# Kernel optimization log

Measured on AMD Instinct MI355X. Metric: run time of the kernel, lower is better.

## Reference

```python
import jax, jax.numpy as jnp
import numpy as np

N, E, G, DIM = 100000, 1600000, 64, 128
BN_EPS = 1e-5


def setup_inputs() -> dict:
    key = jax.random.key(0)
    ks = jax.random.split(key, 20)
    inp = {
        "x": jax.random.normal(ks[0], (N, DIM), jnp.float32),
        "edge_attr": jax.random.normal(ks[1], (E, DIM), jnp.float32),
        "u": jax.random.normal(ks[2], (G, DIM), jnp.float32),
        "edge_index": jax.random.randint(ks[3], (2, E), 0, N, jnp.int32),
        "batch": jnp.sort(jax.random.randint(ks[4], (N,), 0, G, jnp.int32)),
    }
    # MLP params: layer 0 is Linear(3*DIM, DIM), layers 1,2 are Linear(DIM, DIM)
    def xavier(k, shape):
        fan_in, fan_out = shape[1], shape[0]
        lim = jnp.sqrt(6.0 / (fan_in + fan_out))
        return jax.random.uniform(k, shape, jnp.float32, -lim, lim)
    inp["W0"] = xavier(ks[5], (DIM, 3 * DIM)); inp["b0"] = jnp.zeros((DIM,), jnp.float32)
    inp["W1"] = xavier(ks[6], (DIM, DIM));     inp["b1"] = jnp.zeros((DIM,), jnp.float32)
    inp["W2"] = xavier(ks[7], (DIM, DIM));     inp["b2"] = jnp.zeros((DIM,), jnp.float32)
    for i in range(3):
        inp[f"g{i}"] = jnp.ones((DIM,), jnp.float32)   # BN gamma
        inp[f"bt{i}"] = jnp.zeros((DIM,), jnp.float32)  # BN beta
    return inp


def _bn(h, gamma, beta):
    # training-mode BatchNorm1d: batch mean, biased variance
    mu = jnp.mean(h, axis=0)
    var = jnp.var(h, axis=0)
    return (h - mu) * jax.lax.rsqrt(var + BN_EPS) * gamma + beta


def reference(x, edge_attr, u, W0, b0, W1, b1, W2, b2,
              g0, bt0, g1, bt1, g2, bt2, edge_index, batch):
    n = x.shape[0]
    src = edge_index[0]
    # scatter_mean(edge_attr, src) -> [N, DIM]
    sums = jax.ops.segment_sum(edge_attr, src, num_segments=n)
    cnt = jax.ops.segment_sum(jnp.ones((edge_attr.shape[0],), edge_attr.dtype),
                              src, num_segments=n)
    v_e = sums / jnp.maximum(cnt, 1.0)[:, None]
    out = jnp.concatenate([x, v_e, u[batch]], axis=1)  # [N, 3*DIM]
    for W, b, g, bt in ((W0, b0, g0, bt0), (W1, b1, g1, bt1), (W2, b2, g2, bt2)):
        out = jax.nn.relu(out @ W.T + b)
        out = _bn(out, g, bt)
        # dropout_rate = 0.0 -> identity
    return out
```

## Files before the change

kernel.cpp:

```cpp
#include <hip/hip_runtime.h>

#define DIMF 128
#define CAP 128

typedef __bf16 bf16x8 __attribute__((ext_vector_type(8)));
typedef float f32x4 __attribute__((ext_vector_type(4)));
typedef float f32x2 __attribute__((ext_vector_type(2)));

__device__ __forceinline__ unsigned short f2bf(float f) {
    union { float f; unsigned u; } v; v.f = f;
    unsigned r = v.u + 0x7FFFu + ((v.u >> 16) & 1u);
    return (unsigned short)(r >> 16);
}
__device__ __forceinline__ float bf2f(unsigned short h) {
    union { unsigned u; float f; } v; v.u = ((unsigned)h) << 16; return v.f;
}

__global__ __launch_bounds__(256) void k_zero_wconv(int* __restrict__ zbase, int zints,
                                                    const float* __restrict__ W, unsigned short* __restrict__ Wb,
                                                    int n4) {
    int idx = blockIdx.x * 256 + threadIdx.x;
    int z0 = idx * 2;
    if (z0 + 1 < zints) {
        *reinterpret_cast<int2*>(zbase + z0) = int2{0, 0};
    } else if (z0 < zints) {
        zbase[z0] = 0;
    }
    if (idx < n4) {
        float4 v = *reinterpret_cast<const float4*>(W + (size_t)idx * 4);
        ushort4 o = { f2bf(v.x), f2bf(v.y), f2bf(v.z), f2bf(v.w) };
        *reinterpret_cast<ushort4*>(Wb + (size_t)idx * 4) = o;
    }
}

__global__ __launch_bounds__(256) void k_fillb(const int* __restrict__ src, int* __restrict__ cnt,
                                               int* __restrict__ order, int E) {
    int e = blockIdx.x * 256 + threadIdx.x;
    if (e < E) {
        int s = src[e];
        int p = atomicAdd(&cnt[s], 1);
        if (p < CAP) order[(size_t)s * CAP + p] = e;
    }
}

__global__ __launch_bounds__(256) void k_gather(const float* __restrict__ ea, const int* __restrict__ order,
                                                const int* __restrict__ cnt,
                                                unsigned short* __restrict__ ve, int n) {
    int node = blockIdx.x * 4 + (threadIdx.x >> 6);
    if (node >= n) return;
    int lane = threadIdx.x & 63;
    int half = lane >> 5;
    int l32 = lane & 31;
    int c = cnt[node];
    if (c > CAP) c = CAP;
    size_t base = (size_t)node * CAP;

    int id0 = (lane < c) ? order[base + lane] : 0;
    int id1 = (c > 64 && lane < c - 64) ? order[base + 64 + lane] : 0;

    int m  = (c > half) ? ((c - half + 1) >> 1) : 0;
    int mu = (c + 1) >> 1;

#define EID(t) ({ int j_ = half + 2 * (t); \
                  (j_ < 64) ? __shfl(id0, j_, 64) : __shfl(id1, j_ - 64, 64); })
#define LDR(eid) __builtin_nontemporal_load(reinterpret_cast<const f32x4*>(ea + (size_t)(eid) * DIMF) + l32)

    f32x4 s = {0.f, 0.f, 0.f, 0.f};
    f32x4 cur[4], nxt[4];
    int tb = mu >> 2;
    if (tb > 0) {
#pragma unroll
        for (int k = 0; k < 4; ++k) cur[k] = LDR(EID(k));
        for (int b = 1; b < tb; ++b) {
#pragma unroll
            for (int k = 0; k < 4; ++k) nxt[k] = LDR(EID(b * 4 + k));
#pragma unroll
            for (int k = 0; k < 4; ++k) {
                int t = (b - 1) * 4 + k;
                if (t < m) s += cur[k];
                cur[k] = nxt[k];
            }
        }
#pragma unroll
        for (int k = 0; k < 4; ++k) {
            int t = (tb - 1) * 4 + k;
            if (t < m) s += cur[k];
        }
    }
    for (int t = tb * 4; t < mu; ++t) {
        f32x4 v = LDR(EID(t));
        if (t < m) s += v;
    }
#undef EID
#undef LDR

    s[0] += __shfl_xor(s[0], 32, 64);
    s[1] += __shfl_xor(s[1], 32, 64);
    s[2] += __shfl_xor(s[2], 32, 64);
    s[3] += __shfl_xor(s[3], 32, 64);

    if (lane < 32) {
        float inv = 1.0f / (float)(c > 1 ? c : 1);
        ushort4 o = { f2bf(s[0] * inv), f2bf(s[1] * inv), f2bf(s[2] * inv), f2bf(s[3] * inv) };
        *reinterpret_cast<ushort4*>(ve + (size_t)node * DIMF + l32 * 4) = o;
    }
}

#define BM 128

__global__ __launch_bounds__(512) void k_gemm0(const float* __restrict__ x,
                                               const unsigned short* __restrict__ ve,
                                               const float* __restrict__ u,
                                               const int* __restrict__ batch,
                                               const unsigned short* __restrict__ W,
                                               const float* __restrict__ bias,
                                               unsigned short* __restrict__ H,
                                               float* __restrict__ st, int rows) {
    __shared__ __align__(16) unsigned short lA[BM][136];
    __shared__ __align__(16) unsigned short lB[DIMF][136];
    __shared__ float sm[DIMF], sq[DIMF];
    __shared__ int sbatch[BM];
    int tid = threadIdx.x;
    int row0 = blockIdx.x * BM;
    if (tid < DIMF) { sm[tid] = 0.f; sq[tid] = 0.f; }
    if (tid < BM) {
        int gr = row0 + tid;
        sbatch[tid] = (gr < rows) ? batch[gr] : 0;
    }

    int lane = tid & 63, wave = tid >> 6;
    int wm = wave >> 1, wn = wave & 1;
    int l15 = lane & 15, l4 = lane >> 4;
    f32x4 acc[2][4] = {};

    int fr = tid >> 5, fc = (tid & 31) * 4;
    int hr = tid >> 4, hc = (tid & 15) * 8;

#pragma unroll
    for (int chunk = 0; chunk < 3; ++chunk) {
        if (chunk == 0) {
#pragma unroll
            for (int i = 0; i < 8; ++i) {
                int r = fr + i * 16;
                int gr = row0 + r;
                float4 v = (gr < rows) ? *reinterpret_cast<const float4*>(x + (size_t)gr * DIMF + fc)
                                       : float4{0.f, 0.f, 0.f, 0.f};
                ushort4 o2 = { f2bf(v.x), f2bf(v.y), f2bf(v.z), f2bf(v.w) };
                *reinterpret_cast<ushort4*>(&lA[r][fc]) = o2;
            }
        } else if (chunk == 1) {
#pragma unroll
            for (int i = 0; i < 4; ++i) {
                int r = hr + i * 32;
                int gr = row0 + r;
                uint4 v = (gr < rows) ? *reinterpret_cast<const uint4*>(ve + (size_t)gr * DIMF + hc)
                                      : uint4{0u, 0u, 0u, 0u};
                *reinterpret_cast<uint4*>(&lA[r][hc]) = v;
            }
        } else {
#pragma unroll
            for (int i = 0; i < 8; ++i) {
                int r = fr + i * 16;
                int gr = row0 + r;
                int b = sbatch[r];
                float4 v = (gr < rows) ? *reinterpret_cast<const float4*>(u + (size_t)b * DIMF + fc)
                                       : float4{0.f, 0.f, 0.f, 0.f};
                ushort4 o2 = { f2bf(v.x), f2bf(v.y), f2bf(v.z), f2bf(v.w) };
                *reinterpret_cast<ushort4*>(&lA[r][fc]) = o2;
            }
        }
#pragma unroll
        for (int i = 0; i < 4; ++i) {
            int r = hr + i * 32;
            uint4 v = *reinterpret_cast<const uint4*>(W + (size_t)r * 384 + chunk * 128 + hc);
            *reinterpret_cast<uint4*>(&lB[r][hc]) = v;
        }
        __syncthreads();
#pragma unroll
        for (int ks = 0; ks < 4; ++ks) {
            bf16x8 af[2], bfr[4];
#pragma unroll
            for (int mi = 0; mi < 2; ++mi)
                af[mi] = *reinterpret_cast<const bf16x8*>(&lA[wm * 32 + mi * 16 + l15][ks * 32 + l4 * 8]);
#pragma unroll
            for (int ni = 0; ni < 4; ++ni)
                bfr[ni] = *reinterpret_cast<const bf16x8*>(&lB[wn * 64 + ni * 16 + l15][ks * 32 + l4 * 8]);
#pragma unroll
            for (int mi = 0; mi < 2; ++mi)
#pragma unroll
                for (int ni = 0; ni < 4; ++ni)
                    acc[mi][ni] = __builtin_amdgcn_mfma_f32_16x16x32_bf16(af[mi], bfr[ni], acc[mi][ni], 0, 0, 0);
        }
        __syncthreads();
    }

#pragma unroll
    for (int mi = 0; mi < 2; ++mi)
#pragma unroll
        for (int ni = 0; ni < 4; ++ni) {
            int c = wn * 64 + ni * 16 + l15;
            float s = 0.f, q = 0.f;
#pragma unroll
            for (int i = 0; i < 4; ++i) {
                int r = row0 + wm * 32 + mi * 16 + l4 * 4 + i;
                if (r < rows) {
                    float z = acc[mi][ni][i] + bias[c];
                    z = fmaxf(z, 0.f);
                    H[(size_t)r * DIMF + c] = f2bf(z);
                    s += z; q += z * z;
                }
            }
            atomicAdd(&sm[c], s);
            atomicAdd(&sq[c], q);
        }
    __syncthreads();
    if (tid < DIMF) { atomicAdd(&st[tid], sm[tid]); atomicAdd(&st[DIMF + tid], sq[tid]); }
}

__global__ __launch_bounds__(512) void k_gemmF(const unsigned short* __restrict__ A,
                                               const float* __restrict__ W,
                                               const float* __restrict__ bn,
                                               const float* __restrict__ stp,
                                               const float* __restrict__ g,
                                               const float* __restrict__ bt,
                                               unsigned short* __restrict__ H,
                                               float* __restrict__ st, int rows) {
    const int K = 128;
    __shared__ __align__(16) unsigned short lA[BM][136];
    __shared__ __align__(16) unsigned short lB[DIMF][136];
    __shared__ float sS[DIMF], sT[DIMF], bb[DIMF], sm[DIMF], sq[DIMF];
    int tid = threadIdx.x;
    int row0 = blockIdx.x * BM;

    if (tid < DIMF) {
        float invn = 1.0f / (float)rows;
        float mu = stp[tid] * invn;
        float var = stp[DIMF + tid] * invn - mu * mu;
        var = var > 0.f ? var : 0.f;
        float sc = rsqrtf(var + 1e-5f) * g[tid];
        sS[tid] = sc;
        sT[tid] = bt[tid] - mu * sc;
        sm[tid] = 0.f; sq[tid] = 0.f;
    }

    int hr = tid >> 4, hc = (tid & 15) * 8;
#pragma unroll
    for (int i = 0; i < 4; ++i) {
        int r = hr + i * 32;
        int gr = row0 + r;
        uint4 v = (gr < rows) ? *reinterpret_cast<const uint4*>(A + (size_t)gr * K + hc)
                              : uint4{0u, 0u, 0u, 0u};
        *reinterpret_cast<uint4*>(&lA[r][hc]) = v;
    }
    __syncthreads();

    int fr = tid >> 5, fc = (tid & 31) * 4;
#pragma unroll
    for (int it = 0; it < 8; ++it) {
        int r = fr + it * 16;
        float4 w = *reinterpret_cast<const float4*>(W + (size_t)r * K + fc);
        ushort4 ob = { f2bf(w.x * sS[fc]), f2bf(w.y * sS[fc + 1]),
                       f2bf(w.z * sS[fc + 2]), f2bf(w.w * sS[fc + 3]) };
        *reinterpret_cast<ushort4*>(&lB[r][fc]) = ob;
        float p = w.x * sT[fc] + w.y * sT[fc + 1] + w.z * sT[fc + 2] + w.w * sT[fc + 3];
#pragma unroll
        for (int m = 16; m > 0; m >>= 1) p += __shfl_xor(p, m, 32);
        if ((tid & 31) == 0) bb[r] = bn[r] + p;
    }
    __syncthreads();

    int lane = tid & 63, wave = tid >> 6;
    int wm = wave >> 1, wn = wave & 1;
    int l15 = lane & 15, l4 = lane >> 4;
    f32x4 acc[2][4] = {};

#pragma unroll
    for (int ks = 0; ks < 4; ++ks) {
        bf16x8 af[2], bfr[4];
#pragma unroll
        for (int mi = 0; mi < 2; ++mi)
            af[mi] = *reinterpret_cast<const bf16x8*>(&lA[wm * 32 + mi * 16 + l15][ks * 32 + l4 * 8]);
#pragma unroll
        for (int ni = 0; ni < 4; ++ni)
            bfr[ni] = *reinterpret_cast<const bf16x8*>(&lB[wn * 64 + ni * 16 + l15][ks * 32 + l4 * 8]);
#pragma unroll
        for (int mi = 0; mi < 2; ++mi)
#pragma unroll
            for (int ni = 0; ni < 4; ++ni)
                acc[mi][ni] = __builtin_amdgcn_mfma_f32_16x16x32_bf16(af[mi], bfr[ni], acc[mi][ni], 0, 0, 0);
    }

#pragma unroll
    for (int mi = 0; mi < 2; ++mi)
#pragma unroll
        for (int ni = 0; ni < 4; ++ni) {
            int c = wn * 64 + ni * 16 + l15;
            float s = 0.f, q = 0.f;
#pragma unroll
            for (int i = 0; i < 4; ++i) {
                int r = row0 + wm * 32 + mi * 16 + l4 * 4 + i;
                if (r < rows) {
                    float z = acc[mi][ni][i] + bb[c];
                    z = fmaxf(z, 0.f);
                    H[(size_t)r * DIMF + c] = f2bf(z);
                    s += z; q += z * z;
                }
            }
            atomicAdd(&sm[c], s);
            atomicAdd(&sq[c], q);
        }
    __syncthreads();
    if (tid < DIMF) { atomicAdd(&st[tid], sm[tid]); atomicAdd(&st[DIMF + tid], sq[tid]); }
}

__global__ __launch_bounds__(256) void k_final(const unsigned short* __restrict__ H, const float* __restrict__ st,
                                               const float* __restrict__ g, const float* __restrict__ bt,
                                               float* __restrict__ out, int n) {
    int idx = blockIdx.x * 256 + threadIdx.x;
    if (idx >= n * 32) return;
    int r = idx >> 5, q = (idx & 31) * 4;
    float invn = 1.0f / (float)n;
    ushort4 h = *reinterpret_cast<const ushort4*>(H + (size_t)r * DIMF + q);
    float hv[4] = { bf2f(h.x), bf2f(h.y), bf2f(h.z), bf2f(h.w) };
    float ov[4];
#pragma unroll
    for (int k = 0; k < 4; ++k) {
        int c = q + k;
        float mu = st[c] * invn;
        float var = st[DIMF + c] * invn - mu * mu;
        var = var > 0.f ? var : 0.f;
        float sc = rsqrtf(var + 1e-5f) * g[c];
        ov[k] = hv[k] * sc + (bt[c] - mu * sc);
    }
    float4 o = { ov[0], ov[1], ov[2], ov[3] };
    *reinterpret_cast<float4*>(out + (size_t)r * DIMF + q) = o;
}

extern "C" void kernel_launch(void* const* d_in, const int* in_sizes, int n_in,
                              void* d_out, int out_size, void* d_ws, size_t ws_size,
                              hipStream_t stream) {
    const float* x   = (const float*)d_in[0];
    const float* ea  = (const float*)d_in[1];
    const float* u   = (const float*)d_in[2];
    const int* eidx  = (const int*)d_in[3];
    const int* batch = (const int*)d_in[4];
    const float* W0  = (const float*)d_in[5];
    const float* b0  = (const float*)d_in[6];
    const float* W1  = (const float*)d_in[7];
    const float* b1  = (const float*)d_in[8];
    const float* W2  = (const float*)d_in[9];
    const float* b2  = (const float*)d_in[10];
    const float* g0  = (const float*)d_in[11];
    const float* bt0 = (const float*)d_in[12];
    const float* g1  = (const float*)d_in[13];
    const float* bt1 = (const float*)d_in[14];
    const float* g2  = (const float*)d_in[15];
    const float* bt2 = (const float*)d_in[16];

    int N = in_sizes[0] / DIMF;
    int E = in_sizes[1] / DIMF;
    const int* src = eidx;

    char* base = (char*)d_ws;
    size_t o = 0;
    auto alloc = [&](size_t sz) { size_t p = o; o = (o + sz + 255) & ~(size_t)255; return p; };
    size_t off_cnt   = alloc((size_t)N * 4);
    size_t off_st    = alloc(3 * 256 * 4);
    size_t off_order = alloc((size_t)N * CAP * 4);
    size_t off_W0b   = alloc((size_t)DIMF * 384 * 2);
    size_t off_ve    = alloc((size_t)N * DIMF * 2);
    size_t off_h0    = alloc((size_t)N * DIMF * 2);
    size_t off_h1    = alloc((size_t)N * DIMF * 2);
    size_t off_h2    = alloc((size_t)N * DIMF * 2);

    int* cnt        = (int*)(base + off_cnt);
    float* st       = (float*)(base + off_st);
    int* order      = (int*)(base + off_order);
    unsigned short* W0b = (unsigned short*)(base + off_W0b);
    unsigned short* ve  = (unsigned short*)(base + off_ve);
    unsigned short* h0  = (unsigned short*)(base + off_h0);
    unsigned short* h1  = (unsigned short*)(base + off_h1);
    unsigned short* h2  = (unsigned short*)(base + off_h2);
    float* outp = (float*)d_out;

    int zints = (int)((off_st + 3 * 256 * 4) / 4);
    int EB = (E + 255) / 256;
    int NQ = (N * 32 + 255) / 256;
    int GB = (N + BM - 1) / BM;
    int GG = (N + 3) / 4;

    k_zero_wconv<<<256, 256, 0, stream>>>((int*)base, zints, W0, W0b, DIMF * 384 / 4);
    k_fillb<<<EB, 256, 0, stream>>>(src, cnt, order, E);
    k_gather<<<GG, 256, 0, stream>>>(ea, order, cnt, ve, N);

    k_gemm0<<<GB, 512, 0, stream>>>(x, ve, u, batch, W0b, b0, h0, st, N);
    k_gemmF<<<GB, 512, 0, stream>>>(h0, W1, b1, st, g0, bt0, h1, st + 256, N);
    k_gemmF<<<GB, 512, 0, stream>>>(h1, W2, b2, st + 256, g1, bt1, h2, st + 512, N);
    k_final<<<NQ, 256, 0, stream>>>(h2, st + 512, g2, bt2, outp, N);
}
```

Baseline: 516.2 us.

## Precompute BN-folded bf16 weights once and read B fragments from global memory

Adds a small k_fold kernel that folds the previous layer's BatchNorm scale and shift into bf16 weights and a fused bias once per layer. Before this, every GEMM block redid that fold. The GEMM kernels no longer stage W in shared memory; each wave loads its B fragments straight from global memory (expected to hit in L2/L1). This cuts LDS use and per-block setup and may raise occupancy, at the cost of two extra kernel launches and possibly uncoalesced global loads of the weights.

After: 547.3 us. 1.06x slower.

```diff
diff --git a/kernel.cpp b/kernel.cpp
--- a/kernel.cpp
+++ b/kernel.cpp
@@ -5,7 +5,6 @@
 
 typedef __bf16 bf16x8 __attribute__((ext_vector_type(8)));
 typedef float f32x4 __attribute__((ext_vector_type(4)));
-typedef float f32x2 __attribute__((ext_vector_type(2)));
 
 __device__ __forceinline__ unsigned short f2bf(float f) {
     union { float f; unsigned u; } v; v.f = f;
@@ -106,6 +105,29 @@
     }
 }
 
+__global__ __launch_bounds__(128) void k_fold(const float* __restrict__ st, const float* __restrict__ g,
+                                              const float* __restrict__ bt, const float* __restrict__ Wn,
+                                              const float* __restrict__ bn, unsigned short* __restrict__ Wb,
+                                              float* __restrict__ bb, int rows) {
+    int r = blockIdx.x;
+    int i = threadIdx.x;
+    float invn = 1.0f / (float)rows;
+    float mu = st[i] * invn;
+    float var = st[DIMF + i] * invn - mu * mu;
+    var = var > 0.f ? var : 0.f;
+    float sc = rsqrtf(var + 1e-5f) * g[i];
+    float t = bt[i] - mu * sc;
+    float w = Wn[(size_t)r * DIMF + i];
+    Wb[(size_t)r * DIMF + i] = f2bf(w * sc);
+    float p = w * t;
+#pragma unroll
+    for (int m = 32; m > 0; m >>= 1) p += __shfl_xor(p, m, 64);
+    __shared__ float red[2];
+    if ((i & 63) == 0) red[i >> 6] = p;
+    __syncthreads();
+    if (i == 0) bb[r] = bn[r] + red[0] + red[1];
+}
+
 #define BM 128
 
 __global__ __launch_bounds__(512) void k_gemm0(const float* __restrict__ x,
@@ -117,7 +139,6 @@
                                                unsigned short* __restrict__ H,
                                                float* __restrict__ st, int rows) {
     __shared__ __align__(16) unsigned short lA[BM][136];
-    __shared__ __align__(16) unsigned short lB[DIMF][136];
     __shared__ float sm[DIMF], sq[DIMF];
     __shared__ int sbatch[BM];
     int tid = threadIdx.x;
@@ -127,6 +148,7 @@
         int gr = row0 + tid;
         sbatch[tid] = (gr < rows) ? batch[gr] : 0;
     }
+    __syncthreads();
 
     int lane = tid & 63, wave = tid >> 6;
     int wm = wave >> 1, wn = wave & 1;
@@ -135,6 +157,7 @@
 
     int fr = tid >> 5, fc = (tid & 31) * 4;
     int hr = tid >> 4, hc = (tid & 15) * 8;
+    const unsigned short* wp = W + (size_t)(wn * 64 + l15) * 384 + l4 * 8;
 
 #pragma unroll
     for (int chunk = 0; chunk < 3; ++chunk) {
@@ -169,22 +192,16 @@
                 *reinterpret_cast<ushort4*>(&lA[r][fc]) = o2;
             }
         }
-#pragma unroll
-        for (int i = 0; i < 4; ++i) {
-            int r = hr + i * 32;
-            uint4 v = *reinterpret_cast<const uint4*>(W + (size_t)r * 384 + chunk * 128 + hc);
-            *reinterpret_cast<uint4*>(&lB[r][hc]) = v;
-        }
         __syncthreads();
 #pragma unroll
         for (int ks = 0; ks < 4; ++ks) {
             bf16x8 af[2], bfr[4];
 #pragma unroll
+            for (int ni = 0; ni < 4; ++ni)
+                bfr[ni] = *reinterpret_cast<const bf16x8*>(wp + (size_t)ni * 16 * 384 + chunk * 128 + ks * 32);
+#pragma unroll
             for (int mi = 0; mi < 2; ++mi)
                 af[mi] = *reinterpret_cast<const bf16x8*>(&lA[wm * 32 + mi * 16 + l15][ks * 32 + l4 * 8]);
-#pragma unroll
-            for (int ni = 0; ni < 4; ++ni)
-                bfr[ni] = *reinterpret_cast<const bf16x8*>(&lB[wn * 64 + ni * 16 + l15][ks * 32 + l4 * 8]);
 #pragma unroll
             for (int mi = 0; mi < 2; ++mi)
 #pragma unroll
@@ -217,31 +234,17 @@
     if (tid < DIMF) { atomicAdd(&st[tid], sm[tid]); atomicAdd(&st[DIMF + tid], sq[tid]); }
 }
 
-__global__ __launch_bounds__(512) void k_gemmF(const unsigned short* __restrict__ A,
-                                               const float* __restrict__ W,
-                                               const float* __restrict__ bn,
-                                               const float* __restrict__ stp,
-                                               const float* __restrict__ g,
-                                               const float* __restrict__ bt,
+__global__ __launch_bounds__(512) void k_gemmN(const unsigned short* __restrict__ A,
+                                               const unsigned short* __restrict__ Wb,
+                                               const float* __restrict__ bb,
                                                unsigned short* __restrict__ H,
                                                float* __restrict__ st, int rows) {
     const int K = 128;
     __shared__ __align__(16) unsigned short lA[BM][136];
-    __shared__ __align__(16) unsigned short lB[DIMF][136];
-    __shared__ float sS[DIMF], sT[DIMF], bb[DIMF], sm[DIMF], sq[DIMF];
+    __shared__ float sm[DIMF], sq[DIMF];
     int tid = threadIdx.x;
     int row0 = blockIdx.x * BM;
-
-    if (tid < DIMF) {
-        float invn = 1.0f / (float)rows;
-        float mu = stp[tid] * invn;
-        float var = stp[DIMF + tid] * invn - mu * mu;
-        var = var > 0.f ? var : 0.f;
-        float sc = rsqrtf(var + 1e-5f) * g[tid];
-        sS[tid] = sc;
-        sT[tid] = bt[tid] - mu * sc;
-        sm[tid] = 0.f; sq[tid] = 0.f;
-    }
+    if (tid < DIMF) { sm[tid] = 0.f; sq[tid] = 0.f; }
 
     int hr = tid >> 4, hc = (tid & 15) * 8;
 #pragma unroll
@@ -254,35 +257,21 @@
     }
     __syncthreads();
 
-    int fr = tid >> 5, fc = (tid & 31) * 4;
-#pragma unroll
-    for (int it = 0; it < 8; ++it) {
-        int r = fr + it * 16;
-        float4 w = *reinterpret_cast<const float4*>(W + (size_t)r * K + fc);
-        ushort4 ob = { f2bf(w.x * sS[fc]), f2bf(w.y * sS[fc + 1]),
-                       f2bf(w.z * sS[fc + 2]), f2bf(w.w * sS[fc + 3]) };
-        *reinterpret_cast<ushort4*>(&lB[r][fc]) = ob;
-        float p = w.x * sT[fc] + w.y * sT[fc + 1] + w.z * sT[fc + 2] + w.w * sT[fc + 3];
-#pragma unroll
-        for (int m = 16; m > 0; m >>= 1) p += __shfl_xor(p, m, 32);
-        if ((tid & 31) == 0) bb[r] = bn[r] + p;
-    }
-    __syncthreads();
-
     int lane = tid & 63, wave = tid >> 6;
     int wm = wave >> 1, wn = wave & 1;
     int l15 = lane & 15, l4 = lane >> 4;
     f32x4 acc[2][4] = {};
+    const unsigned short* wp = Wb + (size_t)(wn * 64 + l15) * K + l4 * 8;
 
 #pragma unroll
     for (int ks = 0; ks < 4; ++ks) {
         bf16x8 af[2], bfr[4];
 #pragma unroll
+        for (int ni = 0; ni < 4; ++ni)
+            bfr[ni] = *reinterpret_cast<const bf16x8*>(wp + (size_t)ni * 16 * K + ks * 32);
+#pragma unroll
         for (int mi = 0; mi < 2; ++mi)
             af[mi] = *reinterpret_cast<const bf16x8*>(&lA[wm * 32 + mi * 16 + l15][ks * 32 + l4 * 8]);
-#pragma unroll
-        for (int ni = 0; ni < 4; ++ni)
-            bfr[ni] = *reinterpret_cast<const bf16x8*>(&lB[wn * 64 + ni * 16 + l15][ks * 32 + l4 * 8]);
 #pragma unroll
         for (int mi = 0; mi < 2; ++mi)
 #pragma unroll
@@ -368,6 +357,10 @@
     size_t off_st    = alloc(3 * 256 * 4);
     size_t off_order = alloc((size_t)N * CAP * 4);
     size_t off_W0b   = alloc((size_t)DIMF * 384 * 2);
+    size_t off_W1b   = alloc((size_t)DIMF * DIMF * 2);
+    size_t off_W2b   = alloc((size_t)DIMF * DIMF * 2);
+    size_t off_b1f   = alloc(DIMF * 4);
+    size_t off_b2f   = alloc(DIMF * 4);
     size_t off_ve    = alloc((size_t)N * DIMF * 2);
     size_t off_h0    = alloc((size_t)N * DIMF * 2);
     size_t off_h1    = alloc((size_t)N * DIMF * 2);
@@ -377,6 +370,10 @@
     float* st       = (float*)(base + off_st);
     int* order      = (int*)(base + off_order);
     unsigned short* W0b = (unsigned short*)(base + off_W0b);
+    unsigned short* W1b = (unsigned short*)(base + off_W1b);
+    unsigned short* W2b = (unsigned short*)(base + off_W2b);
+    float* b1f      = (float*)(base + off_b1f);
+    float* b2f      = (float*)(base + off_b2f);
     unsigned short* ve  = (unsigned short*)(base + off_ve);
     unsigned short* h0  = (unsigned short*)(base + off_h0);
     unsigned short* h1  = (unsigned short*)(base + off_h1);
@@ -394,7 +391,9 @@
     k_gather<<<GG, 256, 0, stream>>>(ea, order, cnt, ve, N);
 
     k_gemm0<<<GB, 512, 0, stream>>>(x, ve, u, batch, W0b, b0, h0, st, N);
-    k_gemmF<<<GB, 512, 0, stream>>>(h0, W1, b1, st, g0, bt0, h1, st + 256, N);
-    k_gemmF<<<GB, 512, 0, stream>>>(h1, W2, b2, st + 256, g1, bt1, h2, st + 512, N);
+    k_fold<<<DIMF, 128, 0, stream>>>(st, g0, bt0, W1, b1, W1b, b1f, N);
+    k_gemmN<<<GB, 512, 0, stream>>>(h0, W1b, b1f, h1, st + 256, N);
+    k_fold<<<DIMF, 128, 0, stream>>>(st + 256, g1, bt1, W2, b2, W2b, b2f, N);
+    k_gemmN<<<GB, 512, 0, stream>>>(h1, W2b, b2f, h2, st + 512, N);
     k_final<<<NQ, 256, 0, stream>>>(h2, st + 512, g2, bt2, outp, N);
 }
```

## Fuse MLP layers and final BN into one persistent cooperative kernel

Applied to the files above, without the earlier changes.

Replaces the three GEMM kernels and the final BatchNorm kernel with a single cooperative, persistent kernel that loops over row tiles and uses grid-wide syncs between layers to wait for the BN statistics. Each block converts the scaled weights for a layer once and reuses them across all its tiles, and per-block statistics are accumulated across tiles before one global atomic per layer. This removes three kernel launches and repeated per-tile weight conversion, at the cost of grid-sync barriers and a grid limited by occupancy.

Measured after the change: 711.0 us. 1.38x slower.

```diff
diff --git a/kernel.cpp b/kernel.cpp
--- a/kernel.cpp
+++ b/kernel.cpp
@@ -1,11 +1,14 @@
 #include <hip/hip_runtime.h>
+#include <hip/hip_cooperative_groups.h>
+
+namespace cg = cooperative_groups;
 
 #define DIMF 128
 #define CAP 128
+#define BM 128
 
 typedef __bf16 bf16x8 __attribute__((ext_vector_type(8)));
 typedef float f32x4 __attribute__((ext_vector_type(4)));
-typedef float f32x2 __attribute__((ext_vector_type(2)));
 
 __device__ __forceinline__ unsigned short f2bf(float f) {
     union { float f; unsigned u; } v; v.f = f;
@@ -106,234 +109,236 @@
     }
 }
 
-#define BM 128
-
-__global__ __launch_bounds__(512) void k_gemm0(const float* __restrict__ x,
-                                               const unsigned short* __restrict__ ve,
-                                               const float* __restrict__ u,
-                                               const int* __restrict__ batch,
-                                               const unsigned short* __restrict__ W,
-                                               const float* __restrict__ bias,
-                                               unsigned short* __restrict__ H,
-                                               float* __restrict__ st, int rows) {
+__global__ __launch_bounds__(512, 4) void k_mlp(
+    const float* __restrict__ x, const unsigned short* __restrict__ ve,
+    const float* __restrict__ u, const int* __restrict__ batch,
+    const unsigned short* __restrict__ W0b, const float* __restrict__ b0,
+    const float* __restrict__ W1, const float* __restrict__ b1,
+    const float* __restrict__ W2, const float* __restrict__ b2,
+    const float* __restrict__ g0, const float* __restrict__ bt0,
+    const float* __restrict__ g1, const float* __restrict__ bt1,
+    const float* __restrict__ g2, const float* __restrict__ bt2,
+    unsigned short* __restrict__ h0, unsigned short* __restrict__ h1,
+    unsigned short* __restrict__ h2, float* __restrict__ st,
+    float* __restrict__ outp, int rows)
+{
+    cg::grid_group grid = cg::this_grid();
     __shared__ __align__(16) unsigned short lA[BM][136];
     __shared__ __align__(16) unsigned short lB[DIMF][136];
-    __shared__ float sm[DIMF], sq[DIMF];
+    __shared__ float sm[DIMF], sq[DIMF], sS[DIMF], sT[DIMF], bbs[DIMF];
     __shared__ int sbatch[BM];
+
     int tid = threadIdx.x;
-    int row0 = blockIdx.x * BM;
-    if (tid < DIMF) { sm[tid] = 0.f; sq[tid] = 0.f; }
-    if (tid < BM) {
-        int gr = row0 + tid;
-        sbatch[tid] = (gr < rows) ? batch[gr] : 0;
-    }
-
     int lane = tid & 63, wave = tid >> 6;
     int wm = wave >> 1, wn = wave & 1;
     int l15 = lane & 15, l4 = lane >> 4;
-    f32x4 acc[2][4] = {};
-
     int fr = tid >> 5, fc = (tid & 31) * 4;
     int hr = tid >> 4, hc = (tid & 15) * 8;
-
-#pragma unroll
-    for (int chunk = 0; chunk < 3; ++chunk) {
-        if (chunk == 0) {
-#pragma unroll
-            for (int i = 0; i < 8; ++i) {
-                int r = fr + i * 16;
-                int gr = row0 + r;
-                float4 v = (gr < rows) ? *reinterpret_cast<const float4*>(x + (size_t)gr * DIMF + fc)
-                                       : float4{0.f, 0.f, 0.f, 0.f};
-                ushort4 o2 = { f2bf(v.x), f2bf(v.y), f2bf(v.z), f2bf(v.w) };
-                *reinterpret_cast<ushort4*>(&lA[r][fc]) = o2;
-            }
-        } else if (chunk == 1) {
+    int nt = (rows + BM - 1) / BM;
+
+    if (tid < DIMF) { sm[tid] = 0.f; sq[tid] = 0.f; }
+    for (int t = blockIdx.x; t < nt; t += gridDim.x) {
+        int row0 = t * BM;
+        if (tid < BM) {
+            int gr = row0 + tid;
+            sbatch[tid] = (gr < rows) ? batch[gr] : 0;
+        }
+        f32x4 acc[2][4] = {};
+#pragma unroll
+        for (int chunk = 0; chunk < 3; ++chunk) {
+            if (chunk == 0) {
+#pragma unroll
+                for (int i = 0; i < 8; ++i) {
+                    int r = fr + i * 16;
+                    int gr = row0 + r;
+                    float4 v = (gr < rows) ? *reinterpret_cast<const float4*>(x + (size_t)gr * DIMF + fc)
+                                           : float4{0.f, 0.f, 0.f, 0.f};
+                    ushort4 o2 = { f2bf(v.x), f2bf(v.y), f2bf(v.z), f2bf(v.w) };
+                    *reinterpret_cast<ushort4*>(&lA[r][fc]) = o2;
+                }
+            } else if (chunk == 1) {
+#pragma unroll
+                for (int i = 0; i < 4; ++i) {
+                    int r = hr + i * 32;
+                    int gr = row0 + r;
+                    uint4 v = (gr < rows) ? *reinterpret_cast<const uint4*>(ve + (size_t)gr * DIMF + hc)
+                                          : uint4{0u, 0u, 0u, 0u};
+                    *reinterpret_cast<uint4*>(&lA[r][hc]) = v;
+                }
+            } else {
+#pragma unroll
+                for (int i = 0; i < 8; ++i) {
+                    int r = fr + i * 16;
+                    int gr = row0 + r;
+                    int b = sbatch[r];
+                    float4 v = (gr < rows) ? *reinterpret_cast<const float4*>(u + (size_t)b * DIMF + fc)
+                                           : float4{0.f, 0.f, 0.f, 0.f};
+                    ushort4 o2 = { f2bf(v.x), f2bf(v.y), f2bf(v.z), f2bf(v.w) };
+                    *reinterpret_cast<ushort4*>(&lA[r][fc]) = o2;
+                }
+            }
+#pragma unroll
+            for (int i = 0; i < 4; ++i) {
+                int r = hr + i * 32;
+                uint4 v = *reinterpret_cast<const uint4*>(W0b + (size_t)r * 384 + chunk * 128 + hc);
+                *reinterpret_cast<uint4*>(&lB[r][hc]) = v;
+            }
+            __syncthreads();
+#pragma unroll
+            for (int ks = 0; ks < 4; ++ks) {
+                bf16x8 af[2], bfr[4];
+#pragma unroll
+                for (int mi = 0; mi < 2; ++mi)
+                    af[mi] = *reinterpret_cast<const bf16x8*>(&lA[wm * 32 + mi * 16 + l15][ks * 32 + l4 * 8]);
+#pragma unroll
+                for (int ni = 0; ni < 4; ++ni)
+                    bfr[ni] = *reinterpret_cast<const bf16x8*>(&lB[wn * 64 + ni * 16 + l15][ks * 32 + l4 * 8]);
+#pragma unroll
+                for (int mi = 0; mi < 2; ++mi)
+#pragma unroll
+                    for (int ni = 0; ni < 4; ++ni)
+                        acc[mi][ni] = __builtin_amdgcn_mfma_f32_16x16x32_bf16(af[mi], bfr[ni], acc[mi][ni], 0, 0, 0);
+            }
+            __syncthreads();
+        }
+#pragma unroll
+        for (int mi = 0; mi < 2; ++mi)
+#pragma unroll
+            for (int ni = 0; ni < 4; ++ni) {
+                int c = wn * 64 + ni * 16 + l15;
+                float s = 0.f, q = 0.f;
+#pragma unroll
+                for (int i = 0; i < 4; ++i) {
+                    int r = row0 + wm * 32 + mi * 16 + l4 * 4 + i;
+                    if (r < rows) {
+                        float z = acc[mi][ni][i] + b0[c];
+                        z = fmaxf(z, 0.f);
+                        h0[(size_t)r * DIMF + c] = f2bf(z);
+                        s += z; q += z * z;
+                    }
+                }
+                atomicAdd(&sm[c], s);
+                atomicAdd(&sq[c], q);
+            }
+        __syncthreads();
+    }
+    if (tid < DIMF) { atomicAdd(&st[tid], sm[tid]); atomicAdd(&st[DIMF + tid], sq[tid]); }
+
+#pragma unroll 1
+    for (int layer = 0; layer < 2; ++layer) {
+        __threadfence();
+        grid.sync();
+        const float* stp = st + layer * 256;
+        const float* g   = (layer == 0) ? g1 : g2;
+        const float* gg  = (layer == 0) ? g0 : g1;
+        const float* bt  = (layer == 0) ? bt0 : bt1;
+        const float* W   = (layer == 0) ? W1 : W2;
+        const float* bn  = (layer == 0) ? b1 : b2;
+        const unsigned short* A = (layer == 0) ? h0 : h1;
+        unsigned short* H = (layer == 0) ? h1 : h2;
+        float* stn = st + (layer + 1) * 256;
+        (void)g;
+
+        if (tid < DIMF) {
+            float invn = 1.0f / (float)rows;
+            float mu = stp[tid] * invn;
+            float var = stp[DIMF + tid] * invn - mu * mu;
+            var = var > 0.f ? var : 0.f;
+            float sc = rsqrtf(var + 1e-5f) * gg[tid];
+            sS[tid] = sc;
+            sT[tid] = bt[tid] - mu * sc;
+            sm[tid] = 0.f; sq[tid] = 0.f;
+        }
+        __syncthreads();
+#pragma unroll
+        for (int it = 0; it < 8; ++it) {
+            int r = fr + it * 16;
+            float4 w = *reinterpret_cast<const float4*>(W + (size_t)r * DIMF + fc);
+            ushort4 ob = { f2bf(w.x * sS[fc]), f2bf(w.y * sS[fc + 1]),
+                           f2bf(w.z * sS[fc + 2]), f2bf(w.w * sS[fc + 3]) };
+            *reinterpret_cast<ushort4*>(&lB[r][fc]) = ob;
+            float p = w.x * sT[fc] + w.y * sT[fc + 1] + w.z * sT[fc + 2] + w.w * sT[fc + 3];
+#pragma unroll
+            for (int m = 16; m > 0; m >>= 1) p += __shfl_xor(p, m, 32);
+            if ((tid & 31) == 0) bbs[r] = bn[r] + p;
+        }
+        __syncthreads();
+
+        for (int t = blockIdx.x; t < nt; t += gridDim.x) {
+            int row0 = t * BM;
 #pragma unroll
             for (int i = 0; i < 4; ++i) {
                 int r = hr + i * 32;
                 int gr = row0 + r;
-                uint4 v = (gr < rows) ? *reinterpret_cast<const uint4*>(ve + (size_t)gr * DIMF + hc)
+                uint4 v = (gr < rows) ? *reinterpret_cast<const uint4*>(A + (size_t)gr * DIMF + hc)
                                       : uint4{0u, 0u, 0u, 0u};
                 *reinterpret_cast<uint4*>(&lA[r][hc]) = v;
             }
-        } else {
-#pragma unroll
-            for (int i = 0; i < 8; ++i) {
-                int r = fr + i * 16;
-                int gr = row0 + r;
-                int b = sbatch[r];
-                float4 v = (gr < rows) ? *reinterpret_cast<const float4*>(u + (size_t)b * DIMF + fc)
-                                       : float4{0.f, 0.f, 0.f, 0.f};
-                ushort4 o2 = { f2bf(v.x), f2bf(v.y), f2bf(v.z), f2bf(v.w) };
-                *reinterpret_cast<ushort4*>(&lA[r][fc]) = o2;
-            }
-        }
-#pragma unroll
-        for (int i = 0; i < 4; ++i) {
-            int r = hr + i * 32;
-            uint4 v = *reinterpret_cast<const uint4*>(W + (size_t)r * 384 + chunk * 128 + hc);
-            *reinterpret_cast<uint4*>(&lB[r][hc]) = v;
-        }
-        __syncthreads();
-#pragma unroll
-        for (int ks = 0; ks < 4; ++ks) {
-            bf16x8 af[2], bfr[4];
+            __syncthreads();
+            f32x4 acc[2][4] = {};
+#pragma unroll
+            for (int ks = 0; ks < 4; ++ks) {
+                bf16x8 af[2], bfr[4];
+#pragma unroll
+                for (int mi = 0; mi < 2; ++mi)
+                    af[mi] = *reinterpret_cast<const bf16x8*>(&lA[wm * 32 + mi * 16 + l15][ks * 32 + l4 * 8]);
+#pragma unroll
+                for (int ni = 0; ni < 4; ++ni)
+                    bfr[ni] = *reinterpret_cast<const bf16x8*>(&lB[wn * 64 + ni * 16 + l15][ks * 32 + l4 * 8]);
+#pragma unroll
+                for (int mi = 0; mi < 2; ++mi)
+#pragma unroll
+                    for (int ni = 0; ni < 4; ++ni)
+                        acc[mi][ni] = __builtin_amdgcn_mfma_f32_16x16x32_bf16(af[mi], bfr[ni], acc[mi][ni], 0, 0, 0);
+            }
 #pragma unroll
             for (int mi = 0; mi < 2; ++mi)
-                af[mi] = *reinterpret_cast<const bf16x8*>(&lA[wm * 32 + mi * 16 + l15][ks * 32 + l4 * 8]);
-#pragma unroll
-            for (int ni = 0; ni < 4; ++ni)
-                bfr[ni] = *reinterpret_cast<const bf16x8*>(&lB[wn * 64 + ni * 16 + l15][ks * 32 + l4 * 8]);
-#pragma unroll
-            for (int mi = 0; mi < 2; ++mi)
-#pragma unroll
-                for (int ni = 0; ni < 4; ++ni)
-                    acc[mi][ni] = __builtin_amdgcn_mfma_f32_16x16x32_bf16(af[mi], bfr[ni], acc[mi][ni], 0, 0, 0);
-        }
-        __syncthreads();
-    }
-
-#pragma unroll
-    for (int mi = 0; mi < 2; ++mi)
-#pragma unroll
-        for (int ni = 0; ni < 4; ++ni) {
-            int c = wn * 64 + ni * 16 + l15;
-            float s = 0.f, q = 0.f;
-#pragma unroll
-            for (int i = 0; i < 4; ++i) {
-                int r = row0 + wm * 32 + mi * 16 + l4 * 4 + i;
-                if (r < rows) {
-                    float z = acc[mi][ni][i] + bias[c];
-                    z = fmaxf(z, 0.f);
-                    H[(size_t)r * DIMF + c] = f2bf(z);
-                    s += z; q += z * z;
+#pragma unroll
+                for (int ni = 0; ni < 4; ++ni) {
+                    int c = wn * 64 + ni * 16 + l15;
+                    float s = 0.f, q = 0.f;
+#pragma unroll
+                    for (int i = 0; i < 4; ++i) {
+                        int r = row0 + wm * 32 + mi * 16 + l4 * 4 + i;
+                        if (r < rows) {
+                            float z = acc[mi][ni][i] + bbs[c];
+                            z = fmaxf(z, 0.f);
+                            H[(size_t)r * DIMF + c] = f2bf(z);
+                            s += z; q += z * z;
+                        }
+                    }
+                    atomicAdd(&sm[c], s);
+                    atomicAdd(&sq[c], q);
                 }
-            }
-            atomicAdd(&sm[c], s);
-            atomicAdd(&sq[c], q);
-        }
-    __syncthreads();
-    if (tid < DIMF) { atomicAdd(&st[tid], sm[tid]); atomicAdd(&st[DIMF + tid], sq[tid]); }
-}
-
-__global__ __launch_bounds__(512) void k_gemmF(const unsigned short* __restrict__ A,
-                                               const float* __restrict__ W,
-                                               const float* __restrict__ bn,
-                                               const float* __restrict__ stp,
-                                               const float* __restrict__ g,
-                                               const float* __restrict__ bt,
-                                               unsigned short* __restrict__ H,
-                                               float* __restrict__ st, int rows) {
-    const int K = 128;
-    __shared__ __align__(16) unsigned short lA[BM][136];
-    __shared__ __align__(16) unsigned short lB[DIMF][136];
-    __shared__ float sS[DIMF], sT[DIMF], bb[DIMF], sm[DIMF], sq[DIMF];
-    int tid = threadIdx.x;
-    int row0 = blockIdx.x * BM;
-
-    if (tid < DIMF) {
+            __syncthreads();
+        }
+        if (tid < DIMF) { atomicAdd(&stn[tid], sm[tid]); atomicAdd(&stn[DIMF + tid], sq[tid]); }
+    }
+
+    __threadfence();
+    grid.sync();
+    {
+        const float* stf = st + 512;
         float invn = 1.0f / (float)rows;
-        float mu = stp[tid] * invn;
-        float var = stp[DIMF + tid] * invn - mu * mu;
-        var = var > 0.f ? var : 0.f;
-        float sc = rsqrtf(var + 1e-5f) * g[tid];
-        sS[tid] = sc;
-        sT[tid] = bt[tid] - mu * sc;
-        sm[tid] = 0.f; sq[tid] = 0.f;
-    }
-
-    int hr = tid >> 4, hc = (tid & 15) * 8;
-#pragma unroll
-    for (int i = 0; i < 4; ++i) {
-        int r = hr + i * 32;
-        int gr = row0 + r;
-        uint4 v = (gr < rows) ? *reinterpret_cast<const uint4*>(A + (size_t)gr * K + hc)
-                              : uint4{0u, 0u, 0u, 0u};
-        *reinterpret_cast<uint4*>(&lA[r][hc]) = v;
-    }
-    __syncthreads();
-
-    int fr = tid >> 5, fc = (tid & 31) * 4;
-#pragma unroll
-    for (int it = 0; it < 8; ++it) {
-        int r = fr + it * 16;
-        float4 w = *reinterpret_cast<const float4*>(W + (size_t)r * K + fc);
-        ushort4 ob = { f2bf(w.x * sS[fc]), f2bf(w.y * sS[fc + 1]),
-                       f2bf(w.z * sS[fc + 2]), f2bf(w.w * sS[fc + 3]) };
-        *reinterpret_cast<ushort4*>(&lB[r][fc]) = ob;
-        float p = w.x * sT[fc] + w.y * sT[fc + 1] + w.z * sT[fc + 2] + w.w * sT[fc + 3];
-#pragma unroll
-        for (int m = 16; m > 0; m >>= 1) p += __shfl_xor(p, m, 32);
-        if ((tid & 31) == 0) bb[r] = bn[r] + p;
-    }
-    __syncthreads();
-
-    int lane = tid & 63, wave = tid >> 6;
-    int wm = wave >> 1, wn = wave & 1;
-    int l15 = lane & 15, l4 = lane >> 4;
-    f32x4 acc[2][4] = {};
-
-#pragma unroll
-    for (int ks = 0; ks < 4; ++ks) {
-        bf16x8 af[2], bfr[4];
-#pragma unroll
-        for (int mi = 0; mi < 2; ++mi)
-            af[mi] = *reinterpret_cast<const bf16x8*>(&lA[wm * 32 + mi * 16 + l15][ks * 32 + l4 * 8]);
-#pragma unroll
-        for (int ni = 0; ni < 4; ++ni)
-            bfr[ni] = *reinterpret_cast<const bf16x8*>(&lB[wn * 64 + ni * 16 + l15][ks * 32 + l4 * 8]);
-#pragma unroll
-        for (int mi = 0; mi < 2; ++mi)
-#pragma unroll
-            for (int ni = 0; ni < 4; ++ni)
-                acc[mi][ni] = __builtin_amdgcn_mfma_f32_16x16x32_bf16(af[mi], bfr[ni], acc[mi][ni], 0, 0, 0);
-    }
-
-#pragma unroll
-    for (int mi = 0; mi < 2; ++mi)
-#pragma unroll
-        for (int ni = 0; ni < 4; ++ni) {
-            int c = wn * 64 + ni * 16 + l15;
-            float s = 0.f, q = 0.f;
-#pragma unroll
-            for (int i = 0; i < 4; ++i) {
-                int r = row0 + wm * 32 + mi * 16 + l4 * 4 + i;
-                if (r < rows) {
-                    float z = acc[mi][ni][i] + bb[c];
-                    z = fmaxf(z, 0.f);
-                    H[(size_t)r * DIMF + c] = f2bf(z);
-                    s += z; q += z * z;
-                }
-            }
-            atomicAdd(&sm[c], s);
-            atomicAdd(&sq[c], q);
-        }
-    __syncthreads();
-    if (tid < DIMF) { atomicAdd(&st[tid], sm[tid]); atomicAdd(&st[DIMF + tid], sq[tid]); }
-}
-
-__global__ __launch_bounds__(256) void k_final(const unsigned short* __restrict__ H, const float* __restrict__ st,
-                                               const float* __restrict__ g, const float* __restrict__ bt,
-                                               float* __restrict__ out, int n) {
-    int idx = blockIdx.x * 256 + threadIdx.x;
-    if (idx >= n * 32) return;
-    int r = idx >> 5, q = (idx & 31) * 4;
-    float invn = 1.0f / (float)n;
-    ushort4 h = *reinterpret_cast<const ushort4*>(H + (size_t)r * DIMF + q);
-    float hv[4] = { bf2f(h.x), bf2f(h.y), bf2f(h.z), bf2f(h.w) };
-    float ov[4];
-#pragma unroll
-    for (int k = 0; k < 4; ++k) {
-        int c = q + k;
-        float mu = st[c] * invn;
-        float var = st[DIMF + c] * invn - mu * mu;
-        var = var > 0.f ? var : 0.f;
-        float sc = rsqrtf(var + 1e-5f) * g[c];
-        ov[k] = hv[k] * sc + (bt[c] - mu * sc);
-    }
-    float4 o = { ov[0], ov[1], ov[2], ov[3] };
-    *reinterpret_cast<float4*>(out + (size_t)r * DIMF + q) = o;
+        int total = rows * 32;
+        for (int idx = blockIdx.x * 512 + tid; idx < total; idx += gridDim.x * 512) {
+            int r = idx >> 5, q = (idx & 31) * 4;
+            ushort4 h = *reinterpret_cast<const ushort4*>(h2 + (size_t)r * DIMF + q);
+            float hv[4] = { bf2f(h.x), bf2f(h.y), bf2f(h.z), bf2f(h.w) };
+            float ov[4];
+#pragma unroll
+            for (int k = 0; k < 4; ++k) {
+                int c = q + k;
+                float mu = stf[c] * invn;
+                float var = stf[DIMF + c] * invn - mu * mu;
+                var = var > 0.f ? var : 0.f;
+                float sc = rsqrtf(var + 1e-5f) * g2[c];
+                ov[k] = hv[k] * sc + (bt2[c] - mu * sc);
+            }
+            float4 o = { ov[0], ov[1], ov[2], ov[3] };
+            *reinterpret_cast<float4*>(outp + (size_t)r * DIMF + q) = o;
+        }
+    }
 }
 
 extern "C" void kernel_launch(void* const* d_in, const int* in_sizes, int n_in,
@@ -385,16 +390,24 @@
 
     int zints = (int)((off_st + 3 * 256 * 4) / 4);
     int EB = (E + 255) / 256;
-    int NQ = (N * 32 + 255) / 256;
-    int GB = (N + BM - 1) / BM;
     int GG = (N + 3) / 4;
 
     k_zero_wconv<<<256, 256, 0, stream>>>((int*)base, zints, W0, W0b, DIMF * 384 / 4);
     k_fillb<<<EB, 256, 0, stream>>>(src, cnt, order, E);
     k_gather<<<GG, 256, 0, stream>>>(ea, order, cnt, ve, N);
 
-    k_gemm0<<<GB, 512, 0, stream>>>(x, ve, u, batch, W0b, b0, h0, st, N);
-    k_gemmF<<<GB, 512, 0, stream>>>(h0, W1, b1, st, g0, bt0, h1, st + 256, N);
-    k_gemmF<<<GB, 512, 0, stream>>>(h1, W2, b2, st + 256, g1, bt1, h2, st + 512, N);
-    k_final<<<NQ, 256, 0, stream>>>(h2, st + 512, g2, bt2, outp, N);
-}
+    int occ = 0;
+    hipOccupancyMaxActiveBlocksPerMultiprocessor(&occ, k_mlp, 512, 0);
+    if (occ < 1) occ = 1;
+    int nt = (N + BM - 1) / BM;
+    int grid = occ * 256;
+    if (grid > nt) grid = nt;
+
+    void* args[] = { (void*)&x, (void*)&ve, (void*)&u, (void*)&batch,
+                     (void*)&W0b, (void*)&b0, (void*)&W1, (void*)&b1,
+                     (void*)&W2, (void*)&b2, (void*)&g0, (void*)&bt0,
+                     (void*)&g1, (void*)&bt1, (void*)&g2, (void*)&bt2,
+                     (void*)&h0, (void*)&h1, (void*)&h2, (void*)&st,
+                     (void*)&outp, (void*)&N };
+    hipLaunchCooperativeKernel((void*)k_mlp, dim3(grid), dim3(512), args, 0, stream);
+}
```
